# Kernel optimization log

Measured on AMD Instinct MI355X. Metric: run time of the kernel, lower is better.

Reference implementation:

```python
import jax, jax.numpy as jnp
import numpy as np

B, S, D, H = 65536, 5, 128, 8  # batch, seq_len(=5, fixed by property_bias), d_model, heads
HD = D // H                     # head_dim = 16


def setup_inputs() -> dict:
    key = jax.random.key(0)
    ks = jax.random.split(key, 9)
    scale = 0.02
    x = jax.random.normal(ks[0], (B, S, D), jnp.float32)
    Wq = jax.random.normal(ks[1], (D, D), jnp.float32) * scale
    Wk = jax.random.normal(ks[2], (D, D), jnp.float32) * scale
    Wv = jax.random.normal(ks[3], (D, D), jnp.float32) * scale
    Wo = jax.random.normal(ks[4], (D, D), jnp.float32) * scale
    bq = jnp.zeros((D,), jnp.float32)
    bk = jnp.zeros((D,), jnp.float32)
    bv = jnp.zeros((D,), jnp.float32)
    bo = jnp.zeros((D,), jnp.float32)
    # property bias init: zeros except head 0 attends to last property (melting point)
    pbias = jnp.zeros((H, S, S), jnp.float32).at[0, :, -1].set(1.0)
    return {"x": x, "Wq": Wq, "bq": bq, "Wk": Wk, "bk": bk,
            "Wv": Wv, "bv": bv, "Wo": Wo, "bo": bo, "pbias": pbias}


def reference(x, Wq, bq, Wk, bk, Wv, bv, Wo, bo, pbias):
    b, s, d = x.shape
    h = pbias.shape[0]
    hd = d // h
    # projections, split into heads: [b, h, s, hd]
    q = (x @ Wq + bq).reshape(b, s, h, hd).transpose(0, 2, 1, 3)
    k = (x @ Wk + bk).reshape(b, s, h, hd).transpose(0, 2, 1, 3)
    v = (x @ Wv + bv).reshape(b, s, h, hd).transpose(0, 2, 1, 3)
    # scaled dot-product scores + additive per-head property bias
    scores = jnp.einsum('bhsd,bhtd->bhst', q, k) / jnp.sqrt(jnp.float32(hd))
    scores = scores + pbias[None]  # broadcast over batch
    attn = jax.nn.softmax(scores, axis=-1)  # dropout p=0.0 (eval) -> identity
    out = jnp.einsum('bhst,bhtd->bhsd', attn, v)
    out = out.transpose(0, 2, 1, 3).reshape(b, s, d)
    return out @ Wo + bo
```

## Files before the change

kernel.cpp:

```cpp
#include <hip/hip_runtime.h>

typedef _Float16 f16;
typedef _Float16 f16x4 __attribute__((ext_vector_type(4)));
typedef _Float16 f16x8 __attribute__((ext_vector_type(8)));
typedef float f32x4 __attribute__((ext_vector_type(4)));

#define NB 65536
#define SEQ 5
#define DM 128
#define NH 8
#define HDIM 16

__device__ __align__(16) f16 g_WT[4][128][128];

__global__ void k_wtrans(const float* __restrict__ Wq, const float* __restrict__ Wk,
                         const float* __restrict__ Wv, const float* __restrict__ Wo) {
    int tid = blockIdx.x * 256 + threadIdx.x;
    int m = tid >> 14;
    int r = tid & 16383;
    int n = r >> 7;
    int k = r & 127;
    const float* W = (m == 0) ? Wq : (m == 1) ? Wk : (m == 2) ? Wv : Wo;
    g_WT[m][n][k] = (f16)W[k * 128 + n];
}

__global__ __launch_bounds__(320, 4)
void k_fused(const float* __restrict__ x, const float* __restrict__ bq,
             const float* __restrict__ bk, const float* __restrict__ bv,
             const float* __restrict__ bo, const float* __restrict__ pbias,
             float* __restrict__ out) {
    __shared__ __align__(16) f16 Wsl[3][16][136];
    __shared__ __align__(16) f16 WoT2[128][32];
    __shared__ __align__(16) f16 Qh[80][16];
    __shared__ __align__(16) f16 Kh[80][16];
    __shared__ __align__(16) f16 Vh[80][16];
    __shared__ __align__(16) f16 AOl[80][32];
    __shared__ float pb_l[200];
    __shared__ float bo_l[128];
    __shared__ float biasl[3][16];

    const int tid  = threadIdx.x;
    const int wave = tid >> 6;
    const int lane = tid & 63;
    const int c    = lane & 15;
    const int g    = lane >> 4;
    const int token0 = blockIdx.x * 80;

    if (tid < 200) pb_l[tid] = pbias[tid];
    if (tid < 128) bo_l[tid] = bo[tid];

    f16x8 afrag[4];
    {
        int arow = token0 + wave * 16 + c;
        const float* xr = x + (size_t)arow * 128 + g * 8;
#pragma unroll
        for (int ks = 0; ks < 4; ++ks) {
            const float* p = xr + ks * 32;
            float4 u0 = *(const float4*)(p);
            float4 u1 = *(const float4*)(p + 4);
            f16x8 a;
            a[0] = (f16)u0.x; a[1] = (f16)u0.y; a[2] = (f16)u0.z; a[3] = (f16)u0.w;
            a[4] = (f16)u1.x; a[5] = (f16)u1.y; a[6] = (f16)u1.z; a[7] = (f16)u1.w;
            afrag[ks] = a;
        }
    }

    f32x4 outacc[8];
#pragma unroll
    for (int i = 0; i < 8; ++i) outacc[i] = (f32x4){0.f, 0.f, 0.f, 0.f};

    for (int h = 0; h < NH; ++h) {
        for (int u = tid; u < 768; u += 320) {
            int m = u >> 8, r = u & 255, c2 = r >> 4, part = r & 15;
            uint4 val = *(const uint4*)&g_WT[m][16 * h + c2][part * 8];
            *(uint4*)&Wsl[m][c2][part * 8] = val;
        }
        if (tid < 48) {
            const float* bsrc = (tid < 16) ? bq : (tid < 32) ? bk : bv;
            biasl[tid >> 4][tid & 15] = bsrc[16 * h + (tid & 15)];
        }
        __syncthreads();

        f32x4 qa = {0, 0, 0, 0}, ka = {0, 0, 0, 0}, va = {0, 0, 0, 0};
#pragma unroll
        for (int ks = 0; ks < 4; ++ks) {
            int off = ks * 32 + g * 8;
            f16x8 wq = *(const f16x8*)&Wsl[0][c][off];
            f16x8 wk = *(const f16x8*)&Wsl[1][c][off];
            f16x8 wv = *(const f16x8*)&Wsl[2][c][off];
            qa = __builtin_amdgcn_mfma_f32_16x16x32_f16(afrag[ks], wq, qa, 0, 0, 0);
            ka = __builtin_amdgcn_mfma_f32_16x16x32_f16(afrag[ks], wk, ka, 0, 0, 0);
            va = __builtin_amdgcn_mfma_f32_16x16x32_f16(afrag[ks], wv, va, 0, 0, 0);
        }
        {
            int r0 = wave * 16 + g * 4;
            float bqv = biasl[0][c], bkv = biasl[1][c], bvv = biasl[2][c];
#pragma unroll
            for (int r = 0; r < 4; ++r) {
                Qh[r0 + r][c] = (f16)(qa[r] + bqv);
                Kh[r0 + r][c] = (f16)(ka[r] + bkv);
                Vh[r0 + r][c] = (f16)(va[r] + bvv);
            }
        }
        __syncthreads();

        {
            int row = tid >> 2, dq = tid & 3;
            int bl = row / 5;
            int qi = row - bl * 5;
            f16x4 qv = *(const f16x4*)&Qh[row][dq * 4];
            float q0 = (float)qv[0], q1 = (float)qv[1], q2 = (float)qv[2], q3 = (float)qv[3];
            float s[5];
#pragma unroll
            for (int j = 0; j < 5; ++j) {
                f16x4 kv = *(const f16x4*)&Kh[bl * 5 + j][dq * 4];
                float part = q0 * (float)kv[0] + q1 * (float)kv[1] +
                             q2 * (float)kv[2] + q3 * (float)kv[3];
                part += __shfl_xor(part, 1);
                part += __shfl_xor(part, 2);
                s[j] = 0.25f * part + pb_l[h * 25 + qi * 5 + j];
            }
            float mx = fmaxf(fmaxf(fmaxf(s[0], s[1]), fmaxf(s[2], s[3])), s[4]);
            float psum = 0.f;
#pragma unroll
            for (int j = 0; j < 5; ++j) { s[j] = __expf(s[j] - mx); psum += s[j]; }
            float inv = 1.0f / psum;
            float o0 = 0, o1 = 0, o2 = 0, o3 = 0;
#pragma unroll
            for (int j = 0; j < 5; ++j) {
                f16x4 vv = *(const f16x4*)&Vh[bl * 5 + j][dq * 4];
                float pj = s[j] * inv;
                o0 += pj * (float)vv[0]; o1 += pj * (float)vv[1];
                o2 += pj * (float)vv[2]; o3 += pj * (float)vv[3];
            }
            f16x4 ov; ov[0] = (f16)o0; ov[1] = (f16)o1; ov[2] = (f16)o2; ov[3] = (f16)o3;
            *(f16x4*)&AOl[row][(h & 1) * 16 + dq * 4] = ov;
        }

        if (h & 1) {
            int h0 = h - 1;
            for (int u = tid; u < 512; u += 320) {
                int n = u >> 2, part = u & 3;
                uint4 val = *(const uint4*)&g_WT[3][n][h0 * 16 + part * 8];
                *(uint4*)&WoT2[n][part * 8] = val;
            }
        }
        __syncthreads();

        if (h & 1) {
            f16x8 af = *(const f16x8*)&AOl[wave * 16 + c][g * 8];
#pragma unroll
            for (int ct = 0; ct < 8; ++ct) {
                f16x8 bf = *(const f16x8*)&WoT2[ct * 16 + c][g * 8];
                outacc[ct] = __builtin_amdgcn_mfma_f32_16x16x32_f16(af, bf, outacc[ct], 0, 0, 0);
            }
        }
    }

    {
        int r0 = wave * 16 + g * 4;
#pragma unroll
        for (int ct = 0; ct < 8; ++ct) {
            int col = ct * 16 + c;
            float bov = bo_l[col];
#pragma unroll
            for (int r = 0; r < 4; ++r) {
                int gtok = token0 + r0 + r;
                out[(size_t)gtok * 128 + col] = outacc[ct][r] + bov;
            }
        }
    }
}

extern "C" void kernel_launch(void* const* d_in, const int* in_sizes, int n_in,
                              void* d_out, int out_size, void* d_ws, size_t ws_size,
                              hipStream_t stream) {
    const float* x     = (const float*)d_in[0];
    const float* Wq    = (const float*)d_in[1];
    const float* bq    = (const float*)d_in[2];
    const float* Wk    = (const float*)d_in[3];
    const float* bk    = (const float*)d_in[4];
    const float* Wv    = (const float*)d_in[5];
    const float* bv    = (const float*)d_in[6];
    const float* Wo    = (const float*)d_in[7];
    const float* bo    = (const float*)d_in[8];
    const float* pbias = (const float*)d_in[9];
    float* out = (float*)d_out;

    k_wtrans<<<dim3(256), dim3(256), 0, stream>>>(Wq, Wk, Wv, Wo);
    k_fused<<<dim3(NB / 16), dim3(320), 0, stream>>>(x, bq, bk, bv, bo, pbias, out);
}
```

Before: 451.9 us.

## Assign one head per wave with register-resident weights and swizzled shared QKV

The fused kernel is restructured so each of 8 waves owns one head (and one output column slice): Q/K/V weights are kept in registers and the weight MFMA operand order is swapped so x becomes the B operand, looping over 5 token tiles. All heads' Q/K/V are staged once in an XOR-swizzled shared buffer, attention is done per row per lane with fdot2, and the output projection reads attention outputs across heads from shared memory, writing float4 stores. This removes the per-head serial loop with its repeated weight staging and multiple block barriers, at the cost of rereading x from global five times per wave and larger shared memory per block.

```diff
diff --git a/kernel.cpp b/kernel.cpp
--- a/kernel.cpp
+++ b/kernel.cpp
@@ -1,15 +1,12 @@
 #include <hip/hip_runtime.h>
 
 typedef _Float16 f16;
+typedef _Float16 f16x2 __attribute__((ext_vector_type(2)));
 typedef _Float16 f16x4 __attribute__((ext_vector_type(4)));
 typedef _Float16 f16x8 __attribute__((ext_vector_type(8)));
 typedef float f32x4 __attribute__((ext_vector_type(4)));
 
 #define NB 65536
-#define SEQ 5
-#define DM 128
-#define NH 8
-#define HDIM 16
 
 __device__ __align__(16) f16 g_WT[4][128][128];
 
@@ -24,151 +21,175 @@
     g_WT[m][n][k] = (f16)W[k * 128 + n];
 }
 
-__global__ __launch_bounds__(320, 4)
+__device__ __forceinline__ f16x2 bc2(unsigned u) {
+    union { unsigned u; f16x2 h; } x; x.u = u; return x.h;
+}
+__device__ __forceinline__ f16x8 cat8(f16x4 lo, f16x4 hi) {
+    f16x8 r;
+    r[0] = lo[0]; r[1] = lo[1]; r[2] = lo[2]; r[3] = lo[3];
+    r[4] = hi[0]; r[5] = hi[1]; r[6] = hi[2]; r[7] = hi[3];
+    return r;
+}
+
+__global__ __launch_bounds__(512, 4)
 void k_fused(const float* __restrict__ x, const float* __restrict__ bq,
              const float* __restrict__ bk, const float* __restrict__ bv,
              const float* __restrict__ bo, const float* __restrict__ pbias,
              float* __restrict__ out) {
-    __shared__ __align__(16) f16 Wsl[3][16][136];
-    __shared__ __align__(16) f16 WoT2[128][32];
-    __shared__ __align__(16) f16 Qh[80][16];
-    __shared__ __align__(16) f16 Kh[80][16];
-    __shared__ __align__(16) f16 Vh[80][16];
-    __shared__ __align__(16) f16 AOl[80][32];
+    __shared__ __align__(16) f16 QKVs[3][8][80][16];
     __shared__ float pb_l[200];
-    __shared__ float bo_l[128];
-    __shared__ float biasl[3][16];
 
     const int tid  = threadIdx.x;
-    const int wave = tid >> 6;
+    const int w    = tid >> 6;
     const int lane = tid & 63;
     const int c    = lane & 15;
     const int g    = lane >> 4;
-    const int token0 = blockIdx.x * 80;
+    const int base = blockIdx.x * 80;
+    const int key_c = (c >> 2) & 3;
 
     if (tid < 200) pb_l[tid] = pbias[tid];
-    if (tid < 128) bo_l[tid] = bo[tid];
-
-    f16x8 afrag[4];
-    {
-        int arow = token0 + wave * 16 + c;
-        const float* xr = x + (size_t)arow * 128 + g * 8;
+
+    f16x8 wA[3][4];
+#pragma unroll
+    for (int ks = 0; ks < 4; ++ks) {
+        wA[0][ks] = *(const f16x8*)&g_WT[0][w * 16 + c][ks * 32 + g * 8];
+        wA[1][ks] = *(const f16x8*)&g_WT[1][w * 16 + c][ks * 32 + g * 8];
+        wA[2][ks] = *(const f16x8*)&g_WT[2][w * 16 + c][ks * 32 + g * 8];
+    }
+    float4 bq4 = *(const float4*)&bq[w * 16 + g * 4];
+    float4 bk4 = *(const float4*)&bk[w * 16 + g * 4];
+    float4 bv4 = *(const float4*)&bv[w * 16 + g * 4];
+
+#pragma unroll 1
+    for (int t = 0; t < 5; ++t) {
+        const float* xr = x + (size_t)(base + t * 16 + c) * 128;
+        f32x4 qa = {0.f, 0.f, 0.f, 0.f}, ka = {0.f, 0.f, 0.f, 0.f}, va = {0.f, 0.f, 0.f, 0.f};
 #pragma unroll
         for (int ks = 0; ks < 4; ++ks) {
-            const float* p = xr + ks * 32;
-            float4 u0 = *(const float4*)(p);
-            float4 u1 = *(const float4*)(p + 4);
-            f16x8 a;
-            a[0] = (f16)u0.x; a[1] = (f16)u0.y; a[2] = (f16)u0.z; a[3] = (f16)u0.w;
-            a[4] = (f16)u1.x; a[5] = (f16)u1.y; a[6] = (f16)u1.z; a[7] = (f16)u1.w;
-            afrag[ks] = a;
+            float4 u0 = *(const float4*)(xr + ks * 32 + g * 8);
+            float4 u1 = *(const float4*)(xr + ks * 32 + g * 8 + 4);
+            f16x8 bx;
+            bx[0] = (f16)u0.x; bx[1] = (f16)u0.y; bx[2] = (f16)u0.z; bx[3] = (f16)u0.w;
+            bx[4] = (f16)u1.x; bx[5] = (f16)u1.y; bx[6] = (f16)u1.z; bx[7] = (f16)u1.w;
+            qa = __builtin_amdgcn_mfma_f32_16x16x32_f16(wA[0][ks], bx, qa, 0, 0, 0);
+            ka = __builtin_amdgcn_mfma_f32_16x16x32_f16(wA[1][ks], bx, ka, 0, 0, 0);
+            va = __builtin_amdgcn_mfma_f32_16x16x32_f16(wA[2][ks], bx, va, 0, 0, 0);
         }
-    }
-
-    f32x4 outacc[8];
-#pragma unroll
-    for (int i = 0; i < 8; ++i) outacc[i] = (f32x4){0.f, 0.f, 0.f, 0.f};
-
-    for (int h = 0; h < NH; ++h) {
-        for (int u = tid; u < 768; u += 320) {
-            int m = u >> 8, r = u & 255, c2 = r >> 4, part = r & 15;
-            uint4 val = *(const uint4*)&g_WT[m][16 * h + c2][part * 8];
-            *(uint4*)&Wsl[m][c2][part * 8] = val;
-        }
-        if (tid < 48) {
-            const float* bsrc = (tid < 16) ? bq : (tid < 32) ? bk : bv;
-            biasl[tid >> 4][tid & 15] = bsrc[16 * h + (tid & 15)];
-        }
-        __syncthreads();
-
-        f32x4 qa = {0, 0, 0, 0}, ka = {0, 0, 0, 0}, va = {0, 0, 0, 0};
-#pragma unroll
-        for (int ks = 0; ks < 4; ++ks) {
-            int off = ks * 32 + g * 8;
-            f16x8 wq = *(const f16x8*)&Wsl[0][c][off];
-            f16x8 wk = *(const f16x8*)&Wsl[1][c][off];
-            f16x8 wv = *(const f16x8*)&Wsl[2][c][off];
-            qa = __builtin_amdgcn_mfma_f32_16x16x32_f16(afrag[ks], wq, qa, 0, 0, 0);
-            ka = __builtin_amdgcn_mfma_f32_16x16x32_f16(afrag[ks], wk, ka, 0, 0, 0);
-            va = __builtin_amdgcn_mfma_f32_16x16x32_f16(afrag[ks], wv, va, 0, 0, 0);
-        }
-        {
-            int r0 = wave * 16 + g * 4;
-            float bqv = biasl[0][c], bkv = biasl[1][c], bvv = biasl[2][c];
-#pragma unroll
-            for (int r = 0; r < 4; ++r) {
-                Qh[r0 + r][c] = (f16)(qa[r] + bqv);
-                Kh[r0 + r][c] = (f16)(ka[r] + bkv);
-                Vh[r0 + r][c] = (f16)(va[r] + bvv);
-            }
-        }
-        __syncthreads();
-
-        {
-            int row = tid >> 2, dq = tid & 3;
-            int bl = row / 5;
-            int qi = row - bl * 5;
-            f16x4 qv = *(const f16x4*)&Qh[row][dq * 4];
-            float q0 = (float)qv[0], q1 = (float)qv[1], q2 = (float)qv[2], q3 = (float)qv[3];
+        int row  = t * 16 + c;
+        int slot = g ^ key_c;
+        f16x4 qh, kh, vh;
+        qh[0] = (f16)(qa[0] + bq4.x); qh[1] = (f16)(qa[1] + bq4.y);
+        qh[2] = (f16)(qa[2] + bq4.z); qh[3] = (f16)(qa[3] + bq4.w);
+        kh[0] = (f16)(ka[0] + bk4.x); kh[1] = (f16)(ka[1] + bk4.y);
+        kh[2] = (f16)(ka[2] + bk4.z); kh[3] = (f16)(ka[3] + bk4.w);
+        vh[0] = (f16)(va[0] + bv4.x); vh[1] = (f16)(va[1] + bv4.y);
+        vh[2] = (f16)(va[2] + bv4.z); vh[3] = (f16)(va[3] + bv4.w);
+        *(f16x4*)&QKVs[0][w][row][slot * 4] = qh;
+        *(f16x4*)&QKVs[1][w][row][slot * 4] = kh;
+        *(f16x4*)&QKVs[2][w][row][slot * 4] = vh;
+    }
+    __syncthreads();
+
+#pragma unroll 1
+    for (int pass = 0; pass < 2; ++pass) {
+        int task = lane + pass * 64;
+        if (task < 80) {
+            int row = task;
+            int b5  = row / 5;
+            int qi  = row - b5 * 5;
+            int kr0 = b5 * 5;
+            int key = (row >> 2) & 3;
+
+            uint2 qw0 = *(const uint2*)&QKVs[0][w][row][(0 ^ key) * 4];
+            uint2 qw1 = *(const uint2*)&QKVs[0][w][row][(1 ^ key) * 4];
+            uint2 qw2 = *(const uint2*)&QKVs[0][w][row][(2 ^ key) * 4];
+            uint2 qw3 = *(const uint2*)&QKVs[0][w][row][(3 ^ key) * 4];
+            f16x2 q0 = bc2(qw0.x), q1 = bc2(qw0.y), q2 = bc2(qw1.x), q3 = bc2(qw1.y);
+            f16x2 q4 = bc2(qw2.x), q5 = bc2(qw2.y), q6 = bc2(qw3.x), q7 = bc2(qw3.y);
+
             float s[5];
 #pragma unroll
             for (int j = 0; j < 5; ++j) {
-                f16x4 kv = *(const f16x4*)&Kh[bl * 5 + j][dq * 4];
-                float part = q0 * (float)kv[0] + q1 * (float)kv[1] +
-                             q2 * (float)kv[2] + q3 * (float)kv[3];
-                part += __shfl_xor(part, 1);
-                part += __shfl_xor(part, 2);
-                s[j] = 0.25f * part + pb_l[h * 25 + qi * 5 + j];
+                int kr = kr0 + j;
+                int kk = (kr >> 2) & 3;
+                uint2 k0 = *(const uint2*)&QKVs[1][w][kr][(0 ^ kk) * 4];
+                uint2 k1 = *(const uint2*)&QKVs[1][w][kr][(1 ^ kk) * 4];
+                uint2 k2 = *(const uint2*)&QKVs[1][w][kr][(2 ^ kk) * 4];
+                uint2 k3 = *(const uint2*)&QKVs[1][w][kr][(3 ^ kk) * 4];
+                float d = 0.f;
+                d = __builtin_amdgcn_fdot2(q0, bc2(k0.x), d, false);
+                d = __builtin_amdgcn_fdot2(q1, bc2(k0.y), d, false);
+                d = __builtin_amdgcn_fdot2(q2, bc2(k1.x), d, false);
+                d = __builtin_amdgcn_fdot2(q3, bc2(k1.y), d, false);
+                d = __builtin_amdgcn_fdot2(q4, bc2(k2.x), d, false);
+                d = __builtin_amdgcn_fdot2(q5, bc2(k2.y), d, false);
+                d = __builtin_amdgcn_fdot2(q6, bc2(k3.x), d, false);
+                d = __builtin_amdgcn_fdot2(q7, bc2(k3.y), d, false);
+                s[j] = d * 0.25f + pb_l[w * 25 + qi * 5 + j];
             }
             float mx = fmaxf(fmaxf(fmaxf(s[0], s[1]), fmaxf(s[2], s[3])), s[4]);
             float psum = 0.f;
 #pragma unroll
             for (int j = 0; j < 5; ++j) { s[j] = __expf(s[j] - mx); psum += s[j]; }
             float inv = 1.0f / psum;
-            float o0 = 0, o1 = 0, o2 = 0, o3 = 0;
+
+            float o[16];
+#pragma unroll
+            for (int i = 0; i < 16; ++i) o[i] = 0.f;
 #pragma unroll
             for (int j = 0; j < 5; ++j) {
-                f16x4 vv = *(const f16x4*)&Vh[bl * 5 + j][dq * 4];
-                float pj = s[j] * inv;
-                o0 += pj * (float)vv[0]; o1 += pj * (float)vv[1];
-                o2 += pj * (float)vv[2]; o3 += pj * (float)vv[3];
+                int kr = kr0 + j;
+                int kk = (kr >> 2) & 3;
+                uint2 v0 = *(const uint2*)&QKVs[2][w][kr][(0 ^ kk) * 4];
+                uint2 v1 = *(const uint2*)&QKVs[2][w][kr][(1 ^ kk) * 4];
+                uint2 v2 = *(const uint2*)&QKVs[2][w][kr][(2 ^ kk) * 4];
+                uint2 v3 = *(const uint2*)&QKVs[2][w][kr][(3 ^ kk) * 4];
+                float p = s[j] * inv;
+                f16x2 a;
+                a = bc2(v0.x); o[0]  += p * (float)a[0]; o[1]  += p * (float)a[1];
+                a = bc2(v0.y); o[2]  += p * (float)a[0]; o[3]  += p * (float)a[1];
+                a = bc2(v1.x); o[4]  += p * (float)a[0]; o[5]  += p * (float)a[1];
+                a = bc2(v1.y); o[6]  += p * (float)a[0]; o[7]  += p * (float)a[1];
+                a = bc2(v2.x); o[8]  += p * (float)a[0]; o[9]  += p * (float)a[1];
+                a = bc2(v2.y); o[10] += p * (float)a[0]; o[11] += p * (float)a[1];
+                a = bc2(v3.x); o[12] += p * (float)a[0]; o[13] += p * (float)a[1];
+                a = bc2(v3.y); o[14] += p * (float)a[0]; o[15] += p * (float)a[1];
             }
-            f16x4 ov; ov[0] = (f16)o0; ov[1] = (f16)o1; ov[2] = (f16)o2; ov[3] = (f16)o3;
-            *(f16x4*)&AOl[row][(h & 1) * 16 + dq * 4] = ov;
+            f16x4 oc;
+            oc[0] = (f16)o[0];  oc[1] = (f16)o[1];  oc[2] = (f16)o[2];  oc[3] = (f16)o[3];
+            *(f16x4*)&QKVs[0][w][row][(0 ^ key) * 4] = oc;
+            oc[0] = (f16)o[4];  oc[1] = (f16)o[5];  oc[2] = (f16)o[6];  oc[3] = (f16)o[7];
+            *(f16x4*)&QKVs[0][w][row][(1 ^ key) * 4] = oc;
+            oc[0] = (f16)o[8];  oc[1] = (f16)o[9];  oc[2] = (f16)o[10]; oc[3] = (f16)o[11];
+            *(f16x4*)&QKVs[0][w][row][(2 ^ key) * 4] = oc;
+            oc[0] = (f16)o[12]; oc[1] = (f16)o[13]; oc[2] = (f16)o[14]; oc[3] = (f16)o[15];
+            *(f16x4*)&QKVs[0][w][row][(3 ^ key) * 4] = oc;
         }
-
-        if (h & 1) {
-            int h0 = h - 1;
-            for (int u = tid; u < 512; u += 320) {
-                int n = u >> 2, part = u & 3;
-                uint4 val = *(const uint4*)&g_WT[3][n][h0 * 16 + part * 8];
-                *(uint4*)&WoT2[n][part * 8] = val;
-            }
+    }
+    __syncthreads();
+
+    f16x8 wo[4];
+#pragma unroll
+    for (int ks = 0; ks < 4; ++ks)
+        wo[ks] = *(const f16x8*)&g_WT[3][w * 16 + c][ks * 32 + g * 8];
+    float4 bo4 = *(const float4*)&bo[w * 16 + g * 4];
+    const int hh_b = g >> 1;
+    const int c0   = (g & 1) * 2;
+#pragma unroll 1
+    for (int t = 0; t < 5; ++t) {
+        int row = t * 16 + c;
+        f32x4 acc = {0.f, 0.f, 0.f, 0.f};
+#pragma unroll
+        for (int ks = 0; ks < 4; ++ks) {
+            int hh = ks * 2 + hh_b;
+            f16x4 lo = *(const f16x4*)&QKVs[0][hh][row][((c0 ^ key_c)) * 4];
+            f16x4 hi = *(const f16x4*)&QKVs[0][hh][row][(((c0 + 1) ^ key_c)) * 4];
+            acc = __builtin_amdgcn_mfma_f32_16x16x32_f16(wo[ks], cat8(lo, hi), acc, 0, 0, 0);
         }
-        __syncthreads();
-
-        if (h & 1) {
-            f16x8 af = *(const f16x8*)&AOl[wave * 16 + c][g * 8];
-#pragma unroll
-            for (int ct = 0; ct < 8; ++ct) {
-                f16x8 bf = *(const f16x8*)&WoT2[ct * 16 + c][g * 8];
-                outacc[ct] = __builtin_amdgcn_mfma_f32_16x16x32_f16(af, bf, outacc[ct], 0, 0, 0);
-            }
-        }
-    }
-
-    {
-        int r0 = wave * 16 + g * 4;
-#pragma unroll
-        for (int ct = 0; ct < 8; ++ct) {
-            int col = ct * 16 + c;
-            float bov = bo_l[col];
-#pragma unroll
-            for (int r = 0; r < 4; ++r) {
-                int gtok = token0 + r0 + r;
-                out[(size_t)gtok * 128 + col] = outacc[ct][r] + bov;
-            }
-        }
+        float4 r;
+        r.x = acc[0] + bo4.x; r.y = acc[1] + bo4.y;
+        r.z = acc[2] + bo4.z; r.w = acc[3] + bo4.w;
+        *(float4*)&out[(size_t)(base + row) * 128 + w * 16 + g * 4] = r;
     }
 }
 
@@ -188,5 +209,5 @@
     float* out = (float*)d_out;
 
     k_wtrans<<<dim3(256), dim3(256), 0, stream>>>(Wq, Wk, Wv, Wo);
-    k_fused<<<dim3(NB / 16), dim3(320), 0, stream>>>(x, bq, bk, bv, bo, pbias, out);
-}
+    k_fused<<<dim3(NB / 16), dim3(512), 0, stream>>>(x, bq, bk, bv, bo, pbias, out);
+}
```

Measured after the change: 438.4 us. -3.0%, faster.
